# Optimization experiments

Hardware: AMD Instinct MI355X
Metric: run time of the kernel (lower is better)

The kernel has to match this reference:

```python
import jax, jax.numpy as jnp
import numpy as np

EPSILON = 0.1
SOFT_WEIGHT = 0.1
SOFT_LAMBDA = 0.2


def setup_inputs() -> dict:
    key = jax.random.key(0)
    k1, k2, k3 = jax.random.split(key, 3)
    B, C, P = 4096, 32000, 50
    inputs = jax.random.normal(k1, (B, C), dtype=jnp.float32)
    targets = jax.random.randint(k2, (B,), 0, C, dtype=jnp.int64)
    all_posvid = jax.random.randint(k3, (B, P), 0, C, dtype=jnp.int64)
    return {"inputs": inputs, "targets": targets, "all_posvid": all_posvid}


def reference(inputs, targets, all_posvid):
    B, C = inputs.shape
    P = all_posvid.shape[1]
    log_probs = jax.nn.log_softmax(inputs, axis=1)  # [B, C]

    # Per-row unique+counts then scatter is equivalent to a batched histogram:
    # soft_targets[i, c] = soft_lambda * count(c in all_posvid[i]) / P
    row_idx = jnp.broadcast_to(jnp.arange(B)[:, None], all_posvid.shape)
    soft_targets = jnp.zeros((B, C), dtype=log_probs.dtype).at[row_idx, all_posvid].add(
        SOFT_LAMBDA / P
    )

    onehot = jax.nn.one_hot(targets, C, dtype=log_probs.dtype)  # [B, C]

    # soft_label=True branch
    soft_targets = (1.0 - SOFT_LAMBDA) * onehot + soft_targets
    smoothed = (1.0 - EPSILON) * onehot + EPSILON / C

    loss_hard = (-smoothed * log_probs).mean(0).sum()
    loss_soft = (-soft_targets * log_probs).mean(0).sum()
    return loss_hard * (1.0 - SOFT_WEIGHT) + loss_soft * SOFT_WEIGHT
```

## Files before the change

### kernel.cpp

```cpp
#include <hip/hip_runtime.h>
#include <math.h>


#define NB 4096
#define NC 32000
#define NP 50

__global__ __launch_bounds__(256) void row_loss_kernel(
    const float* __restrict__ x,
    const int*   __restrict__ targets,
    const int*   __restrict__ posvid,
    float*       __restrict__ row_loss)
{
    const int row = blockIdx.x;
    const int tid = threadIdx.x;
    const float* __restrict__ xr = x + (size_t)row * NC;
    const float4* __restrict__ x4 = (const float4*)xr;

    float e0 = 0.0f, e1 = 0.0f, e2 = 0.0f, e3 = 0.0f;
    float t0 = 0.0f, t1 = 0.0f, t2 = 0.0f, t3 = 0.0f;

#pragma unroll 2
    for (int idx = tid; idx < NC / 4; idx += 256) {
        float4 v = x4[idx];
        e0 += __expf(v.x);
        e1 += __expf(v.y);
        e2 += __expf(v.z);
        e3 += __expf(v.w);
        t0 += v.x;
        t1 += v.y;
        t2 += v.z;
        t3 += v.w;
    }

    float s    = (e0 + e1) + (e2 + e3);
    float sumx = (t0 + t1) + (t2 + t3);

    __shared__ float ss[256];
    __shared__ float sx[256];
    ss[tid] = s; sx[tid] = sumx;
    __syncthreads();

    for (int off = 128; off > 0; off >>= 1) {
        if (tid < off) {
            ss[tid] += ss[tid + off];
            sx[tid] += sx[tid + off];
        }
        __syncthreads();
    }

    float g = 0.0f;
    if (tid < NP) {
        int c = posvid[(size_t)row * NP + tid];
        g = xr[c];
    }
    if (tid < 64) {
#pragma unroll
        for (int off = 32; off > 0; off >>= 1)
            g += __shfl_down(g, off, 64);
    }

    if (tid == 0) {
        const float EPSILON     = 0.1f;
        const float SOFT_WEIGHT = 0.1f;
        const float SOFT_LAMBDA = 0.2f;
        const float A  = (1.0f - SOFT_WEIGHT) * (1.0f - EPSILON)
                       + SOFT_WEIGHT * (1.0f - SOFT_LAMBDA);
        const float C1 = (1.0f - SOFT_WEIGHT) * EPSILON / (float)NC;
        const float C2 = SOFT_WEIGHT * SOFT_LAMBDA / (float)NP;

        float lse  = logf(ss[0]);
        float sxt  = sx[0];
        float xt   = xr[targets[row]];
        float loss = -( A  * (xt  - lse)
                      + C1 * (sxt - (float)NC * lse)
                      + C2 * (g   - (float)NP * lse) );
        row_loss[row] = loss;
    }
}

__global__ __launch_bounds__(256) void reduce_kernel(
    const float* __restrict__ rl, float* __restrict__ out)
{
    __shared__ float sm[256];
    const int tid = threadIdx.x;
    float acc = 0.0f;
    for (int i = tid; i < NB; i += 256)
        acc += rl[i];
    sm[tid] = acc;
    __syncthreads();
    for (int off = 128; off > 0; off >>= 1) {
        if (tid < off) sm[tid] += sm[tid + off];
        __syncthreads();
    }
    if (tid == 0) out[0] = sm[0] * (1.0f / (float)NB);
}

extern "C" void kernel_launch(void* const* d_in, const int* in_sizes, int n_in,
                              void* d_out, int out_size, void* d_ws, size_t ws_size,
                              hipStream_t stream)
{
    const float* x       = (const float*)d_in[0];
    const int*   targets = (const int*)d_in[1];
    const int*   posvid  = (const int*)d_in[2];
    float*       out     = (float*)d_out;
    float*       ws      = (float*)d_ws;

    row_loss_kernel<<<NB, 256, 0, stream>>>(x, targets, posvid, ws);
    reduce_kernel<<<1, 256, 0, stream>>>(ws, out);
}
```

Baseline: 101.3 us.

## Fuse final reduction into row kernel via last-block atomic counter; use nontemporal loads

Replaces the separate single-block reduce kernel with a last-block-done pattern: each block atomically increments a counter, and the final block sums all row losses and writes the output. A memset of the counter is added to the stream. Row loads switch to nontemporal builtin loads to avoid cache pollution on the streamed input. This removes one kernel launch in exchange for a memset plus an atomic per block and a serialized tail reduction in one block.

```diff
diff --git a/kernel.cpp b/kernel.cpp
--- a/kernel.cpp
+++ b/kernel.cpp
@@ -6,23 +6,27 @@
 #define NC 32000
 #define NP 50
 
-__global__ __launch_bounds__(256) void row_loss_kernel(
+typedef float f4 __attribute__((ext_vector_type(4)));
+
+__global__ __launch_bounds__(256) void fused_loss_kernel(
     const float* __restrict__ x,
     const int*   __restrict__ targets,
     const int*   __restrict__ posvid,
-    float*       __restrict__ row_loss)
+    float*       __restrict__ row_loss,
+    unsigned int* __restrict__ counter,
+    float*       __restrict__ out)
 {
     const int row = blockIdx.x;
     const int tid = threadIdx.x;
     const float* __restrict__ xr = x + (size_t)row * NC;
-    const float4* __restrict__ x4 = (const float4*)xr;
+    const f4*    __restrict__ x4 = (const f4*)xr;
 
     float e0 = 0.0f, e1 = 0.0f, e2 = 0.0f, e3 = 0.0f;
     float t0 = 0.0f, t1 = 0.0f, t2 = 0.0f, t3 = 0.0f;
 
 #pragma unroll 2
     for (int idx = tid; idx < NC / 4; idx += 256) {
-        float4 v = x4[idx];
+        f4 v = __builtin_nontemporal_load(x4 + idx);
         e0 += __expf(v.x);
         e1 += __expf(v.y);
         e2 += __expf(v.z);
@@ -70,30 +74,34 @@
         const float C2 = SOFT_WEIGHT * SOFT_LAMBDA / (float)NP;
 
         float lse  = logf(ss[0]);
-        float sxt  = sx[0];
-        float xt   = xr[targets[row]];
-        float loss = -( A  * (xt  - lse)
-                      + C1 * (sxt - (float)NC * lse)
-                      + C2 * (g   - (float)NP * lse) );
+        float loss = -( A  * (xr[targets[row]] - lse)
+                      + C1 * (sx[0] - (float)NC * lse)
+                      + C2 * (g     - (float)NP * lse) );
         row_loss[row] = loss;
     }
-}
 
-__global__ __launch_bounds__(256) void reduce_kernel(
-    const float* __restrict__ rl, float* __restrict__ out)
-{
-    __shared__ float sm[256];
-    const int tid = threadIdx.x;
-    float acc = 0.0f;
-    for (int i = tid; i < NB; i += 256)
-        acc += rl[i];
-    sm[tid] = acc;
+    __shared__ int is_last;
+    if (tid == 0) {
+        unsigned int old = __hip_atomic_fetch_add(counter, 1u,
+                                                  __ATOMIC_ACQ_REL,
+                                                  __HIP_MEMORY_SCOPE_AGENT);
+        is_last = (old == NB - 1) ? 1 : 0;
+    }
     __syncthreads();
-    for (int off = 128; off > 0; off >>= 1) {
-        if (tid < off) sm[tid] += sm[tid + off];
+
+    if (is_last) {
+        __threadfence();
+        float acc = 0.0f;
+        for (int i = tid; i < NB; i += 256)
+            acc += row_loss[i];
+        ss[tid] = acc;
         __syncthreads();
+        for (int off = 128; off > 0; off >>= 1) {
+            if (tid < off) ss[tid] += ss[tid + off];
+            __syncthreads();
+        }
+        if (tid == 0) out[0] = ss[0] * (1.0f / (float)NB);
     }
-    if (tid == 0) out[0] = sm[0] * (1.0f / (float)NB);
 }
 
 extern "C" void kernel_launch(void* const* d_in, const int* in_sizes, int n_in,
@@ -104,8 +112,9 @@
     const int*   targets = (const int*)d_in[1];
     const int*   posvid  = (const int*)d_in[2];
     float*       out     = (float*)d_out;
-    float*       ws      = (float*)d_ws;
+    float*       rl      = (float*)d_ws;
+    unsigned int* counter = (unsigned int*)(rl + NB);
 
-    row_loss_kernel<<<NB, 256, 0, stream>>>(x, targets, posvid, ws);
-    reduce_kernel<<<1, 256, 0, stream>>>(ws, out);
+    hipMemsetAsync(counter, 0, sizeof(unsigned int), stream);
+    fused_loss_kernel<<<NB, 256, 0, stream>>>(x, targets, posvid, rl, counter, out);
 }
```

Result: slower. 276.7 us (+173.2%).
